# Optimization experiments

Hardware: AMD Instinct MI355X
Metric: run time of the kernel (lower is better)

## Reference

```python
import jax, jax.numpy as jnp
import numpy as np

# Module config (matches init_kwargs)
G, K, S = 64, 3, 2          # base patch size, num scales, scale factor
B, H, W, C = 64, 512, 512, 3
HG, HL = 128, 128
D_IN = K * G * G * C


def setup_inputs() -> dict:
    key = jax.random.key(0)
    kx, kl, k1, k2 = jax.random.split(key, 4)
    x = jax.random.normal(kx, (B, H, W, C), dtype=jnp.float32)
    # glimpse locations in [-1, 1)
    l = jax.random.uniform(kl, (B, 2), minval=-1.0, maxval=1.0, dtype=jnp.float32)
    # fc1: phi (D_IN -> HG); fc2: l (2 -> HL). PyTorch-Linear-like scale.
    W1 = jax.random.normal(k1, (D_IN, HG), dtype=jnp.float32) / np.sqrt(D_IN)
    b1 = jnp.zeros((HG,), dtype=jnp.float32)
    W2 = jax.random.normal(k2, (2, HL), dtype=jnp.float32) / np.sqrt(2.0)
    b2 = jnp.zeros((HL,), dtype=jnp.float32)
    return {"x": x, "l": l, "W1": W1, "b1": b1, "W2": W2, "b2": b2}


def _extract_glimpse(x, l):
    """Retina: k multi-scale patches centered at l, resized to (G,G).
    Returns (B, K, G, G, C)."""
    sizes = [G * S**i for i in range(K)]              # 64, 128, 256
    pad = sizes[-1] // 2 + 1                          # pad once for largest scale
    xp = jnp.pad(x, ((0, 0), (pad, pad), (pad, pad), (0, 0)))
    # denormalize: [-1,1] -> [0,H], truncated to int (torch .long())
    coords = (0.5 * (l + 1.0) * H).astype(jnp.int32)  # (B,2): col0=x, col1=y
    patches = []
    for size in sizes:
        fy = coords[:, 1] - size // 2 + pad
        fx = coords[:, 0] - size // 2 + pad

        def slice_one(img, y0, x0, size=size):
            return jax.lax.dynamic_slice(img, (y0, x0, 0), (size, size, C))

        p = jax.vmap(slice_one)(xp, fy, fx)           # (B, size, size, C)
        f = size // G
        if f > 1:  # downsample by integer factor via average pooling
            p = p.reshape(B, G, f, G, f, C).mean(axis=(2, 4))
        patches.append(p)
    return jnp.stack(patches, axis=1)                 # (B, K, G, G, C)


def reference(x, l, W1, b1, W2, b2):
    phi = _extract_glimpse(x, l).reshape(x.shape[0], -1)   # (B, K*G*G*C)
    phi_out = jax.nn.relu(phi @ W1 + b1)                   # (B, HG)
    l_out = jax.nn.relu(l @ W2 + b2)                       # (B, HL)
    return jax.nn.relu(jnp.concatenate([phi_out, l_out], axis=1))
```

## Files before the change

### kernel.cpp

```cpp
#include <hip/hip_runtime.h>

#define G_     64
#define NK     3
#define NB     64
#define IH     512
#define IW     512
#define NC     3
#define HG_    128
#define HL_    128
#define D_IN_    (NK * G_ * G_ * NC)
#define D_SCALE  (G_ * G_ * NC)
#define KCH      128
#define NCHUNK   (D_IN_ / KCH)
#define BSPLIT   8
#define NBLK     (NCHUNK * BSPLIT)
#define PSTRIDE  (NB * HG_)

template <int F>
__device__ __forceinline__ void scale_body(
    const float* __restrict__ x, const float* __restrict__ l,
    const float* __restrict__ W1, float* __restrict__ P,
    int roff, int d0, int b0, int chunkGlobal,
    float (&phi_s)[8][KCH], float (&red2)[3][8][HG_], int* cx_s, int* cy_s)
{
    const int tid = threadIdx.x;
    if (tid < 8) {
        float lx = l[(b0 + tid) * 2 + 0];
        float ly = l[(b0 + tid) * 2 + 1];
        cx_s[tid] = (int)((0.5f * (lx + 1.0f)) * 512.0f);
        cy_s[tid] = (int)((0.5f * (ly + 1.0f)) * 512.0f);
    }
    __syncthreads();

    const int dd   = tid & (KCH - 1);
    const int jb0  = (tid >> 7) * 4;
    const int r    = roff + dd;
    const int gy   = r / (G_ * NC);
    const int rem  = r - gy * (G_ * NC);
    const int gx   = rem / NC;
    const int c    = rem - gx * NC;
    constexpr float inv = 1.0f / (float)(F * F);
    constexpr int JU = (F == 4) ? 2 : 4;

#pragma unroll 1
    for (int jo = 0; jo < 4; jo += JU) {
        float sums[JU];
#pragma unroll
        for (int ji = 0; ji < JU; ++ji) {
            const int jb = jb0 + jo + ji;
            const int b  = b0 + jb;
            const int by = cy_s[jb] - 32 * F + gy * F;
            const int bx = cx_s[jb] - 32 * F + gx * F;
            const float* bimg = x + (size_t)b * (IH * IW * NC) + c;
            float s = 0.0f;
#pragma unroll
            for (int dy = 0; dy < F; ++dy) {
                const int y = by + dy;
                const bool yok = (unsigned)y < (unsigned)IH;
#pragma unroll
                for (int dx = 0; dx < F; ++dx) {
                    const int xx = bx + dx;
                    const bool ok = yok && ((unsigned)xx < (unsigned)IW);
                    s += ok ? bimg[(size_t)y * (IW * NC) + xx * NC] : 0.0f;
                }
            }
            sums[ji] = s;
        }
#pragma unroll
        for (int ji = 0; ji < JU; ++ji)
            phi_s[jb0 + jo + ji][dd] = sums[ji] * inv;
    }
    __syncthreads();

    const int hq  = tid & 31;
    const int h0  = hq * 4;
    const int gg  = tid >> 5;
    const int bg4 = (gg & 1) * 4;
    const int dq  = gg >> 1;
    const int db  = dq * 32;

    float4 a0 = {0.f, 0.f, 0.f, 0.f};
    float4 a1 = {0.f, 0.f, 0.f, 0.f};
    float4 a2 = {0.f, 0.f, 0.f, 0.f};
    float4 a3 = {0.f, 0.f, 0.f, 0.f};
    const float* wp = W1 + (size_t)(d0 + db) * HG_ + h0;

#pragma unroll 1
    for (int t = 0; t < 8; ++t) {
        const float4 pv0 = *(const float4*)&phi_s[bg4 + 0][db + 4 * t];
        const float4 pv1 = *(const float4*)&phi_s[bg4 + 1][db + 4 * t];
        const float4 pv2 = *(const float4*)&phi_s[bg4 + 2][db + 4 * t];
        const float4 pv3 = *(const float4*)&phi_s[bg4 + 3][db + 4 * t];
#pragma unroll
        for (int u = 0; u < 4; ++u) {
            const float4 wv = *(const float4*)(wp + (size_t)(4 * t + u) * HG_);
            const float p0 = (&pv0.x)[u];
            const float p1 = (&pv1.x)[u];
            const float p2 = (&pv2.x)[u];
            const float p3 = (&pv3.x)[u];
            a0.x = fmaf(p0, wv.x, a0.x); a0.y = fmaf(p0, wv.y, a0.y);
            a0.z = fmaf(p0, wv.z, a0.z); a0.w = fmaf(p0, wv.w, a0.w);
            a1.x = fmaf(p1, wv.x, a1.x); a1.y = fmaf(p1, wv.y, a1.y);
            a1.z = fmaf(p1, wv.z, a1.z); a1.w = fmaf(p1, wv.w, a1.w);
            a2.x = fmaf(p2, wv.x, a2.x); a2.y = fmaf(p2, wv.y, a2.y);
            a2.z = fmaf(p2, wv.z, a2.z); a2.w = fmaf(p2, wv.w, a2.w);
            a3.x = fmaf(p3, wv.x, a3.x); a3.y = fmaf(p3, wv.y, a3.y);
            a3.z = fmaf(p3, wv.z, a3.z); a3.w = fmaf(p3, wv.w, a3.w);
        }
    }

    if (dq != 0) {
        *(float4*)&red2[dq - 1][bg4 + 0][h0] = a0;
        *(float4*)&red2[dq - 1][bg4 + 1][h0] = a1;
        *(float4*)&red2[dq - 1][bg4 + 2][h0] = a2;
        *(float4*)&red2[dq - 1][bg4 + 3][h0] = a3;
    }
    __syncthreads();
    if (dq == 0) {
        float* pb = P + (size_t)chunkGlobal * PSTRIDE + (size_t)(b0 + bg4) * HG_ + h0;
#pragma unroll
        for (int q = 0; q < 3; ++q) {
            const float4 r0 = *(const float4*)&red2[q][bg4 + 0][h0];
            const float4 r1 = *(const float4*)&red2[q][bg4 + 1][h0];
            const float4 r2 = *(const float4*)&red2[q][bg4 + 2][h0];
            const float4 r3 = *(const float4*)&red2[q][bg4 + 3][h0];
            a0.x += r0.x; a0.y += r0.y; a0.z += r0.z; a0.w += r0.w;
            a1.x += r1.x; a1.y += r1.y; a1.z += r1.z; a1.w += r1.w;
            a2.x += r2.x; a2.y += r2.y; a2.z += r2.z; a2.w += r2.w;
            a3.x += r3.x; a3.y += r3.y; a3.z += r3.z; a3.w += r3.w;
        }
        *(float4*)(pb + 0 * HG_) = a0;
        *(float4*)(pb + 1 * HG_) = a1;
        *(float4*)(pb + 2 * HG_) = a2;
        *(float4*)(pb + 3 * HG_) = a3;
    }
}

__global__ __launch_bounds__(256, 8) void fused(
    const float* __restrict__ x, const float* __restrict__ l,
    const float* __restrict__ W1, float* __restrict__ P)
{
    __shared__ float phi_s[8][KCH];
    __shared__ float red2[3][8][HG_];
    __shared__ int cx_s[8], cy_s[8];

    const int cg = blockIdx.x >> 3;
    const int b0 = (blockIdx.x & 7) * 8;

    if (cg < 96) {
        const int cl = cg;
        scale_body<4>(x, l, W1, P, cl * KCH, 2 * D_SCALE + cl * KCH, b0, cg,
                      phi_s, red2, cx_s, cy_s);
    } else if (cg < 192) {
        const int cl = cg - 96;
        scale_body<2>(x, l, W1, P, cl * KCH, D_SCALE + cl * KCH, b0, cg,
                      phi_s, red2, cx_s, cy_s);
    } else {
        const int cl = cg - 192;
        scale_body<1>(x, l, W1, P, cl * KCH, cl * KCH, b0, cg,
                      phi_s, red2, cx_s, cy_s);
    }
}

__global__ __launch_bounds__(256) void reduce_epilogue(
    const float* __restrict__ P,
    const float* __restrict__ l,
    const float* __restrict__ b1,
    const float* __restrict__ W2,
    const float* __restrict__ b2,
    float* __restrict__ out)
{
    __shared__ float4 red[32][8];
    const int b    = blockIdx.x >> 2;
    const int q    = blockIdx.x & 3;
    const int t    = threadIdx.x;
    const int lane = t & 7;
    const int grp  = t >> 3;

    const float4* p4 = (const float4*)P
                     + (size_t)(grp * 9) * (PSTRIDE / 4)
                     + (size_t)b * (HG_ / 4) + q * 8 + lane;
    float4 a = make_float4(0.f, 0.f, 0.f, 0.f);
#pragma unroll
    for (int i = 0; i < 9; ++i) {
        const float4 v = p4[(size_t)i * (PSTRIDE / 4)];
        a.x += v.x; a.y += v.y; a.z += v.z; a.w += v.w;
    }
    red[grp][lane] = a;
    __syncthreads();

#pragma unroll
    for (int s = 16; s >= 1; s >>= 1) {
        if (grp < s) {
            const float4 o = red[grp + s][lane];
            float4 m = red[grp][lane];
            m.x += o.x; m.y += o.y; m.z += o.z; m.w += o.w;
            red[grp][lane] = m;
        }
        __syncthreads();
    }

    if (t < 8) {
        const float4 a2 = red[0][t];
        const float4 bb = ((const float4*)b1)[q * 8 + t];
        float4 o;
        o.x = fmaxf(a2.x + bb.x, 0.0f);
        o.y = fmaxf(a2.y + bb.y, 0.0f);
        o.z = fmaxf(a2.z + bb.z, 0.0f);
        o.w = fmaxf(a2.w + bb.w, 0.0f);
        ((float4*)out)[(size_t)b * ((HG_ + HL_) / 4) + q * 8 + t] = o;
    } else if (t >= 64 && t < 96) {
        const int h = q * 32 + (t - 64);
        const float l0 = l[b * 2 + 0];
        const float l1 = l[b * 2 + 1];
        const float v = fmaf(l1, W2[HL_ + h], fmaf(l0, W2[h], b2[h]));
        out[(size_t)b * (HG_ + HL_) + HG_ + h] = fmaxf(v, 0.0f);
    }
}

extern "C" void kernel_launch(void* const* d_in, const int* in_sizes, int n_in,
                              void* d_out, int out_size, void* d_ws, size_t ws_size,
                              hipStream_t stream) {
    const float* x  = (const float*)d_in[0];
    const float* l  = (const float*)d_in[1];
    const float* W1 = (const float*)d_in[2];
    const float* b1 = (const float*)d_in[3];
    const float* W2 = (const float*)d_in[4];
    const float* b2 = (const float*)d_in[5];
    float* out = (float*)d_out;
    float* P = (float*)d_ws;

    fused<<<NBLK, 256, 0, stream>>>(x, l, W1, P);
    reduce_epilogue<<<NB * 4, 256, 0, stream>>>(P, l, b1, W2, b2, out);
}
```

Measured before the change: 279.6 us.

## Remap GEMV threads to cover all eight batch rows and reduce in two stages

Each thread now accumulates all 8 batch rows over 16 reduction elements instead of 4 rows over 32. Each loaded W1 float4 is therefore reused across 8 rows, which halves per-block W1 global traffic. The cross-group reduction becomes a two-stage shared-memory tree with an extra barrier and a larger scratch buffer. Occupancy hint drops from 8 to 6 blocks per SIMD to fit the larger register accumulator set.

```diff
diff --git a/kernel.cpp b/kernel.cpp
--- a/kernel.cpp
+++ b/kernel.cpp
@@ -21,7 +21,7 @@
     const float* __restrict__ x, const float* __restrict__ l,
     const float* __restrict__ W1, float* __restrict__ P,
     int roff, int d0, int b0, int chunkGlobal,
-    float (&phi_s)[8][KCH], float (&red2)[3][8][HG_], int* cx_s, int* cy_s)
+    float (&phi_s)[8][KCH], float4 (&scr)[4][8][HG_ / 4], int* cx_s, int* cy_s)
 {
     const int tid = threadIdx.x;
     if (tid < 8) {
@@ -72,76 +72,85 @@
     }
     __syncthreads();
 
-    const int hq  = tid & 31;
-    const int h0  = hq * 4;
-    const int gg  = tid >> 5;
-    const int bg4 = (gg & 1) * 4;
-    const int dq  = gg >> 1;
-    const int db  = dq * 32;
-
-    float4 a0 = {0.f, 0.f, 0.f, 0.f};
-    float4 a1 = {0.f, 0.f, 0.f, 0.f};
-    float4 a2 = {0.f, 0.f, 0.f, 0.f};
-    float4 a3 = {0.f, 0.f, 0.f, 0.f};
-    const float* wp = W1 + (size_t)(d0 + db) * HG_ + h0;
+    const int hq    = tid & 31;
+    const int h0    = hq * 4;
+    const int dg    = tid >> 5;
+    const int dbase = dg * 16;
+
+    float4 acc[8];
+#pragma unroll
+    for (int b = 0; b < 8; ++b) acc[b] = make_float4(0.f, 0.f, 0.f, 0.f);
+
+    const float* wp = W1 + (size_t)(d0 + dbase) * HG_ + h0;
 
 #pragma unroll 1
-    for (int t = 0; t < 8; ++t) {
-        const float4 pv0 = *(const float4*)&phi_s[bg4 + 0][db + 4 * t];
-        const float4 pv1 = *(const float4*)&phi_s[bg4 + 1][db + 4 * t];
-        const float4 pv2 = *(const float4*)&phi_s[bg4 + 2][db + 4 * t];
-        const float4 pv3 = *(const float4*)&phi_s[bg4 + 3][db + 4 * t];
-#pragma unroll
-        for (int u = 0; u < 4; ++u) {
-            const float4 wv = *(const float4*)(wp + (size_t)(4 * t + u) * HG_);
-            const float p0 = (&pv0.x)[u];
-            const float p1 = (&pv1.x)[u];
-            const float p2 = (&pv2.x)[u];
-            const float p3 = (&pv3.x)[u];
-            a0.x = fmaf(p0, wv.x, a0.x); a0.y = fmaf(p0, wv.y, a0.y);
-            a0.z = fmaf(p0, wv.z, a0.z); a0.w = fmaf(p0, wv.w, a0.w);
-            a1.x = fmaf(p1, wv.x, a1.x); a1.y = fmaf(p1, wv.y, a1.y);
-            a1.z = fmaf(p1, wv.z, a1.z); a1.w = fmaf(p1, wv.w, a1.w);
-            a2.x = fmaf(p2, wv.x, a2.x); a2.y = fmaf(p2, wv.y, a2.y);
-            a2.z = fmaf(p2, wv.z, a2.z); a2.w = fmaf(p2, wv.w, a2.w);
-            a3.x = fmaf(p3, wv.x, a3.x); a3.y = fmaf(p3, wv.y, a3.y);
-            a3.z = fmaf(p3, wv.z, a3.z); a3.w = fmaf(p3, wv.w, a3.w);
-        }
-    }
-
-    if (dq != 0) {
-        *(float4*)&red2[dq - 1][bg4 + 0][h0] = a0;
-        *(float4*)&red2[dq - 1][bg4 + 1][h0] = a1;
-        *(float4*)&red2[dq - 1][bg4 + 2][h0] = a2;
-        *(float4*)&red2[dq - 1][bg4 + 3][h0] = a3;
-    }
-    __syncthreads();
-    if (dq == 0) {
-        float* pb = P + (size_t)chunkGlobal * PSTRIDE + (size_t)(b0 + bg4) * HG_ + h0;
-#pragma unroll
-        for (int q = 0; q < 3; ++q) {
-            const float4 r0 = *(const float4*)&red2[q][bg4 + 0][h0];
-            const float4 r1 = *(const float4*)&red2[q][bg4 + 1][h0];
-            const float4 r2 = *(const float4*)&red2[q][bg4 + 2][h0];
-            const float4 r3 = *(const float4*)&red2[q][bg4 + 3][h0];
-            a0.x += r0.x; a0.y += r0.y; a0.z += r0.z; a0.w += r0.w;
-            a1.x += r1.x; a1.y += r1.y; a1.z += r1.z; a1.w += r1.w;
-            a2.x += r2.x; a2.y += r2.y; a2.z += r2.z; a2.w += r2.w;
-            a3.x += r3.x; a3.y += r3.y; a3.z += r3.z; a3.w += r3.w;
-        }
-        *(float4*)(pb + 0 * HG_) = a0;
-        *(float4*)(pb + 1 * HG_) = a1;
-        *(float4*)(pb + 2 * HG_) = a2;
-        *(float4*)(pb + 3 * HG_) = a3;
-    }
-}
-
-__global__ __launch_bounds__(256, 8) void fused(
+    for (int t4 = 0; t4 < 4; ++t4) {
+        const float4 wv0 = *(const float4*)(wp + (size_t)(4 * t4 + 0) * HG_);
+        const float4 wv1 = *(const float4*)(wp + (size_t)(4 * t4 + 1) * HG_);
+        const float4 wv2 = *(const float4*)(wp + (size_t)(4 * t4 + 2) * HG_);
+        const float4 wv3 = *(const float4*)(wp + (size_t)(4 * t4 + 3) * HG_);
+#pragma unroll
+        for (int b = 0; b < 8; ++b) {
+            const float4 pv = *(const float4*)&phi_s[b][dbase + 4 * t4];
+            acc[b].x = fmaf(pv.x, wv0.x, acc[b].x);
+            acc[b].y = fmaf(pv.x, wv0.y, acc[b].y);
+            acc[b].z = fmaf(pv.x, wv0.z, acc[b].z);
+            acc[b].w = fmaf(pv.x, wv0.w, acc[b].w);
+            acc[b].x = fmaf(pv.y, wv1.x, acc[b].x);
+            acc[b].y = fmaf(pv.y, wv1.y, acc[b].y);
+            acc[b].z = fmaf(pv.y, wv1.z, acc[b].z);
+            acc[b].w = fmaf(pv.y, wv1.w, acc[b].w);
+            acc[b].x = fmaf(pv.z, wv2.x, acc[b].x);
+            acc[b].y = fmaf(pv.z, wv2.y, acc[b].y);
+            acc[b].z = fmaf(pv.z, wv2.z, acc[b].z);
+            acc[b].w = fmaf(pv.z, wv2.w, acc[b].w);
+            acc[b].x = fmaf(pv.w, wv3.x, acc[b].x);
+            acc[b].y = fmaf(pv.w, wv3.y, acc[b].y);
+            acc[b].z = fmaf(pv.w, wv3.z, acc[b].z);
+            acc[b].w = fmaf(pv.w, wv3.w, acc[b].w);
+        }
+    }
+
+    if (dg >= 4) {
+#pragma unroll
+        for (int b = 0; b < 8; ++b) scr[dg - 4][b][hq] = acc[b];
+    }
+    __syncthreads();
+    if (dg < 4) {
+#pragma unroll
+        for (int b = 0; b < 8; ++b) {
+            const float4 rv = scr[dg][b][hq];
+            acc[b].x += rv.x; acc[b].y += rv.y;
+            acc[b].z += rv.z; acc[b].w += rv.w;
+        }
+    }
+    __syncthreads();
+    if (dg >= 1 && dg < 4) {
+#pragma unroll
+        for (int b = 0; b < 8; ++b) scr[dg - 1][b][hq] = acc[b];
+    }
+    __syncthreads();
+    if (dg == 0) {
+        float* pb = P + (size_t)chunkGlobal * PSTRIDE + (size_t)b0 * HG_ + h0;
+#pragma unroll
+        for (int b = 0; b < 8; ++b) {
+#pragma unroll
+            for (int q = 0; q < 3; ++q) {
+                const float4 rv = scr[q][b][hq];
+                acc[b].x += rv.x; acc[b].y += rv.y;
+                acc[b].z += rv.z; acc[b].w += rv.w;
+            }
+            *(float4*)(pb + (size_t)b * HG_) = acc[b];
+        }
+    }
+}
+
+__global__ __launch_bounds__(256, 6) void fused(
     const float* __restrict__ x, const float* __restrict__ l,
     const float* __restrict__ W1, float* __restrict__ P)
 {
     __shared__ float phi_s[8][KCH];
-    __shared__ float red2[3][8][HG_];
+    __shared__ float4 scr[4][8][HG_ / 4];
     __shared__ int cx_s[8], cy_s[8];
 
     const int cg = blockIdx.x >> 3;
@@ -150,15 +159,15 @@
     if (cg < 96) {
         const int cl = cg;
         scale_body<4>(x, l, W1, P, cl * KCH, 2 * D_SCALE + cl * KCH, b0, cg,
-                      phi_s, red2, cx_s, cy_s);
+                      phi_s, scr, cx_s, cy_s);
     } else if (cg < 192) {
         const int cl = cg - 96;
         scale_body<2>(x, l, W1, P, cl * KCH, D_SCALE + cl * KCH, b0, cg,
-                      phi_s, red2, cx_s, cy_s);
+                      phi_s, scr, cx_s, cy_s);
     } else {
         const int cl = cg - 192;
         scale_body<1>(x, l, W1, P, cl * KCH, cl * KCH, b0, cg,
-                      phi_s, red2, cx_s, cy_s);
+                      phi_s, scr, cx_s, cy_s);
     }
 }
 
```

New measurement: 275.5 us. About the same (-1.4%).
